# Optimization experiments

Hardware: AMD Instinct MI355X
Metric: run time of the kernel (lower is better)

The kernel has to match this reference:

```python
import jax, jax.numpy as jnp
import numpy as np

N = 100_000   # nodes
E = 3_200_000 # directed edges (avg degree 32)
D = 256       # feature dim (in_channels)
K = 2         # k of k-MIS


def _propagate_min(min_rank, row, col, n, k):
    # k iterations of scatter_min along edges (row -> col), keeping current value
    for _ in range(k):
        neigh = jax.ops.segment_min(min_rank[row], col, num_segments=n)
        min_rank = jnp.minimum(min_rank, neigh)
    return min_rank


def maximal_k_independent_set(row, col, rank, n, k):
    # Luby-style greedy k-MIS: repeatedly add nodes whose rank is minimal in their
    # k-hop in-neighbourhood, then mark (cover) the k-hop neighbourhood of the MIS.
    def dilate(mask):
        for _ in range(k):
            neigh = jax.ops.segment_max(mask[row].astype(jnp.int32), col, num_segments=n)
            mask = mask | (neigh > 0)
        return mask

    def cond(state):
        _, mask, _ = state
        return ~jnp.all(mask)

    def body(state):
        mis, mask, min_rank = state
        min_rank = _propagate_min(min_rank, row, col, n, k)
        mis = mis | (rank == min_rank)
        mask = dilate(mis)
        min_rank = jnp.where(mask, n, rank)  # covered nodes get rank 'infinity' (= n)
        return mis, mask, min_rank

    z = jnp.zeros((n,), dtype=bool)
    mis, _, _ = jax.lax.while_loop(cond, body, (z, z, rank))
    return mis


def cluster_k_mis(mis, row, col, rank, n, k):
    # min_rank = n everywhere except MIS nodes get their rank; propagate min k hops;
    # cluster id = index of the unique MIS rank each node ends up attached to.
    min_rank = jnp.where(mis, rank, n)
    min_rank = _propagate_min(min_rank, row, col, n, k)
    _, clusters = jnp.unique(min_rank, return_inverse=True)
    return clusters.reshape(-1).astype(jnp.int32)


def setup_inputs():
    key = jax.random.key(0)
    k1, k2, k3 = jax.random.split(key, 3)
    x = jax.random.normal(k1, (N, D), dtype=jnp.float32)
    edge_index = jax.random.randint(k2, (2, E), 0, N, dtype=jnp.int32)
    edge_attr = jax.random.normal(k3, (E,), dtype=jnp.float32)
    return {"x": x, "edge_index": edge_index, "edge_attr": edge_attr}


def reference(x, edge_index, edge_attr):
    n = x.shape[0]
    row, col = edge_index[0], edge_index[1]
    # scorer=None -> score = arange(n); greedy ordering of arange -> rank = arange(n)
    rank = jnp.arange(n, dtype=jnp.int32)

    mis = maximal_k_independent_set(row, col, rank, n, K)
    cluster = cluster_k_mis(mis, row, col, rank, n, K)
    c = int(mis.sum())  # number of clusters (MIS size)

    # --- pooled adjacency: coalesce duplicate (cluster[row], cluster[col]) with sum ---
    cl_np = np.asarray(cluster).astype(np.int64)
    r = cl_np[np.asarray(row)]
    cc = cl_np[np.asarray(col)]
    keys = r * np.int64(c) + cc
    uniq, inv = np.unique(keys, return_inverse=True)
    val = jax.ops.segment_sum(edge_attr, jnp.asarray(inv.astype(np.int32)),
                              num_segments=int(uniq.shape[0]))
    new_row = (uniq // c).astype(np.int32)
    new_col = (uniq % c).astype(np.int32)
    keep = np.nonzero(new_row != new_col)[0]  # remove_self_loops=True
    pooled_edge_index = jnp.stack([jnp.asarray(new_row[keep]), jnp.asarray(new_col[keep])])
    pooled_edge_attr = val[jnp.asarray(keep)]

    # --- pooled node features: reduce_x='sum' (adaptive=False, so no score scaling) ---
    x_pooled = jax.ops.segment_sum(x, cluster, num_segments=c)
    return x_pooled, pooled_edge_index, pooled_edge_attr
```

## Files before the change

kernel.cpp:

```cpp
#include <hip/hip_runtime.h>
#include <cmath>
#include <cstdint>

#define NT 256
#define EG0 1024
#define EG1 256
#define MAX_ROUND 16
#define KCOPY 4
#define SCAN_T 32
#define SCAN_IPB (NT*SCAN_T)
#define SENT 0x80000000u


__device__ __forceinline__ int getbit(const unsigned int* bm, int v){
  return (bm[v>>5]>>(v&31))&1u;
}
__device__ __forceinline__ void setbit(unsigned int* bm, int v){
  unsigned int m = 1u<<(v&31);
  if(!(bm[v>>5]&m)) atomicOr(&bm[v>>5], m);
}

__device__ __forceinline__ int block_append(int* cursor, bool pred, int* s_w){
  int wid  = threadIdx.x >> 6;
  int lane = threadIdx.x & 63;
  unsigned long long m = __ballot(pred);
  int cnt = __popcll(m);
  if(lane==0) s_w[wid]=cnt;
  __syncthreads();
  if(threadIdx.x==0){
    int t0=s_w[0], t1=s_w[1], t2=s_w[2], t3=s_w[3];
    int tot=t0+t1+t2+t3;
    int base = tot ? atomicAdd(cursor, tot) : 0;
    s_w[0]=base; s_w[1]=base+t0; s_w[2]=base+t0+t1; s_w[3]=base+t0+t1+t2;
  }
  __syncthreads();
  int pos = s_w[wid] + __popcll(m & ((1ull<<lane)-1ull));
  __syncthreads();
  return pos;
}


__global__ void k_init(int* a, int* b, int n){
  int v = blockIdx.x*NT + threadIdx.x;
  if(v<n){ a[v]=v; b[v]=v; }
}

__global__ void k_fill_dense(float* dcopies, const int* scal, long CMsq){
  long c = scal[0];
  long M = c*c; if(M>CMsq) M=CMsq;
  long stride = (long)gridDim.x*NT;
  for(long i = (long)blockIdx.x*NT + threadIdx.x; i<M; i+=stride){
    #pragma unroll
    for(int k=0;k<KCOPY;k++)
      ((unsigned int*)dcopies)[(long)k*CMsq + i] = SENT;
  }
}


__global__ void k_hop0(int* b, const int* __restrict__ row,
                       const int* __restrict__ col, int E){
  int stride = gridDim.x*NT;
  for(int e = blockIdx.x*NT + threadIdx.x; e<E; e+=stride){
    int s = row[e];
    if(s < b[col[e]]) atomicMin(&b[col[e]], s);
  }
}

__global__ void k_hop0f(int* a, const int* b, const int* __restrict__ row,
                        const int* __restrict__ col, int n, int E){
  int stride = gridDim.x*NT;
  int total = n + E;
  for(int i = blockIdx.x*NT + threadIdx.x; i<total; i+=stride){
    if(i<n){
      if(b[i] < a[i]) atomicMin(&a[i], b[i]);
    } else {
      int e = i-n;
      int s = b[row[e]];
      if(s < a[col[e]]) atomicMin(&a[col[e]], s);
    }
  }
}

__global__ void k_dil0(const int* a, int* d2, int* cover, const int* __restrict__ row,
                       const int* __restrict__ col, int E, int ep){
  int stride = gridDim.x*NT;
  for(int e = blockIdx.x*NT + threadIdx.x; e<E; e+=stride){
    int r = row[e];
    if(a[r]==r){
      int cc = col[e];
      d2[r]=ep;  cover[r]=1;
      d2[cc]=ep; cover[cc]=1;
    }
  }
}

__global__ void k_dil20(const int* a, const int* d2, int* cover, const int* __restrict__ row,
                        const int* __restrict__ col, int E, int ep){
  int stride = gridDim.x*NT;
  for(int e = blockIdx.x*NT + threadIdx.x; e<E; e+=stride){
    int r = row[e];
    if((d2[r]==ep || a[r]==r) && !cover[col[e]]) cover[col[e]]=1;
  }
}

__global__ void k_fincomp0(int* a, int* b, unsigned int* misb, int* cover, int n,
                           const int* __restrict__ row, const int* __restrict__ col, int E,
                           int2* Ld, int* lcnt1, int* U1, int* rcnt0){
  __shared__ int s_w[4];
  long nth = (long)gridDim.x*NT;
  for(long base = (long)blockIdx.x*NT; base < n; base += nth){
    int v = (int)base + threadIdx.x;
    bool unc = false;
    if(v<n){
      int nw = (a[v]==v);
      if(nw){ setbit(misb,v); if(!cover[v]) cover[v]=1; }
      int cov = cover[v] | nw;
      int val = cov ? n : v;
      a[v]=val; b[v]=val;
      unc = !cov;
    }
    int pos = block_append(rcnt0, unc, s_w);
    if(unc) U1[pos]=v;
  }
  for(long base = (long)blockIdx.x*NT; base < E; base += nth){
    int e = (int)base + threadIdx.x;
    bool keep=false; int2 ed;
    if(e<E){
      ed = make_int2(row[e], col[e]);
      keep = (!cover[ed.x]) || (!cover[ed.y]);
    }
    int pos = block_append(lcnt1, keep, s_w);
    if(keep) Ld[pos]=ed;
  }
}


__global__ void k_hop1(int* b, const int* a, const int2* L, const int* pE,
                       const int* gate){
  if(*gate==0) return;
  int E = *pE;
  int stride = gridDim.x*NT;
  for(int e = blockIdx.x*NT + threadIdx.x; e<E; e+=stride){
    int2 ed = L[e];
    int s = a[ed.x];
    if(s < b[ed.y]) atomicMin(&b[ed.y], s);
  }
}

__global__ void k_hop1f(int* a, const int* b, const int2* L, const int* pE,
                        const int* U, const int* pU, const int* gate){
  if(*gate==0) return;
  int E = *pE, un = *pU;
  int total = un + E;
  int stride = gridDim.x*NT;
  for(int i = blockIdx.x*NT + threadIdx.x; i<total; i+=stride){
    if(i<un){
      int u = U[i];
      if(b[u] < a[u]) atomicMin(&a[u], b[u]);
    } else {
      int2 ed = L[i-un];
      int s = b[ed.x];
      if(s < a[ed.y]) atomicMin(&a[ed.y], s);
    }
  }
}

__global__ void k_dil11(const int* a, int* d2, int* cover, unsigned int* misb,
                        const int2* L, const int* pE, const int* U, const int* pU,
                        const int* gate, int ep){
  if(*gate==0) return;
  int E = *pE, un = *pU;
  int total = un + E;
  int stride = gridDim.x*NT;
  for(int i = blockIdx.x*NT + threadIdx.x; i<total; i+=stride){
    if(i<un){
      int u = U[i];
      if(a[u]==u){ setbit(misb,u); cover[u]=1; d2[u]=ep; }
    } else {
      int2 ed = L[i-un];
      if(a[ed.x]==ed.x){ d2[ed.x]=ep; cover[ed.x]=1; d2[ed.y]=ep; cover[ed.y]=1; }
    }
  }
}

__global__ void k_dil21(const int* a, const int* d2, int* cover, const int2* L,
                        const int* pE, const int* gate, int ep){
  if(*gate==0) return;
  int E = *pE;
  int stride = gridDim.x*NT;
  for(int e = blockIdx.x*NT + threadIdx.x; e<E; e+=stride){
    int2 ed = L[e];
    if((d2[ed.x]==ep || a[ed.x]==ed.x) && !cover[ed.y]) cover[ed.y]=1;
  }
}

__global__ void k_fincomp1(int* a, int* b, const int* cover, int n,
                           const int2* Ls, const int* pE, int2* Ld, int* lcntD,
                           const int* Us, const int* pU, int* Ud, int* rcntD,
                           const int* gate){
  if(*gate==0) return;
  __shared__ int s_w[4];
  int E = *pE, un = *pU;
  long nth = (long)gridDim.x*NT;
  for(long base = (long)blockIdx.x*NT; base < un; base += nth){
    int i = (int)base + threadIdx.x;
    bool unc=false; int u=0;
    if(i<un){ u = Us[i]; unc = !cover[u]; }
    int pos = block_append(rcntD, unc, s_w);
    if(unc) Ud[pos]=u;
  }
  for(long base = (long)blockIdx.x*NT; base < E; base += nth){
    int e = (int)base + threadIdx.x;
    bool keep=false; int2 ed;
    if(e<E){
      ed = Ls[e];
      int vx = cover[ed.x] ? n : ed.x;  a[ed.x]=vx; b[ed.x]=vx;
      int vy = cover[ed.y] ? n : ed.y;  a[ed.y]=vy; b[ed.y]=vy;
      keep = (!cover[ed.x]) || (!cover[ed.y]);
    }
    int pos = block_append(lcntD, keep, s_w);
    if(keep) Ld[pos]=ed;
  }
}


__global__ void k_cluster_init(const unsigned int* misb, unsigned int* reach1b,
                               int* a, int* b, int n){
  int v = blockIdx.x*NT + threadIdx.x;
  if(v<n){
    int m = getbit(misb,v);
    int val = m ? v : n;
    a[v]=val; b[v]=val;
    if(m) setbit(reach1b,v);
  }
}

__global__ void k_chop1(int* b, const unsigned int* misb, unsigned int* reach1b,
                        const int* __restrict__ row, const int* __restrict__ col, int E){
  int stride = gridDim.x*NT;
  for(int e = blockIdx.x*NT + threadIdx.x; e<E; e+=stride){
    int r = row[e];
    if(getbit(misb,r)){
      int cc = col[e];
      if(r < b[cc]) atomicMin(&b[cc], r);
      setbit(reach1b, cc);
    }
  }
}

__global__ void k_chop2f(int* a, const int* b, const unsigned int* reach1b,
                         const int* __restrict__ row, const int* __restrict__ col,
                         int n, int E){
  int stride = gridDim.x*NT;
  int total = n + E;
  for(int i = blockIdx.x*NT + threadIdx.x; i<total; i+=stride){
    if(i<n){
      if(b[i] < a[i]) atomicMin(&a[i], b[i]);
    } else {
      int e = i-n;
      int r = row[e];
      if(getbit(reach1b,r)){
        int s = b[r];
        if(s < n && s < a[col[e]]) atomicMin(&a[col[e]], s);
      }
    }
  }
}

__global__ void k_mark(const int* mr, const unsigned int* misb, int* present, int* cmis, int n){
  int v = blockIdx.x*NT + threadIdx.x;
  int m = 0;
  if(v<n){
    int r = mr[v];
    if(r<n && !present[r]) present[r]=1;
    m = getbit(misb,v);
  }
  __shared__ int sh[NT];
  sh[threadIdx.x]=m; __syncthreads();
  for(int off=NT/2; off>0; off>>=1){
    if(threadIdx.x<off) sh[threadIdx.x]+=sh[threadIdx.x+off];
    __syncthreads();
  }
  if(threadIdx.x==0 && sh[0]) atomicAdd(cmis, sh[0]);
}


__global__ void k_scan1(const int* A, int M, int* bsum){
  int t = threadIdx.x;
  long base = (long)blockIdx.x*SCAN_IPB + (long)t*SCAN_T;
  int s = 0;
  #pragma unroll
  for(int j=0;j<SCAN_T;j++){ long i=base+j; if(i<M) s += A[i]; }
  __shared__ int sh[NT];
  sh[t]=s; __syncthreads();
  for(int off=NT/2; off>0; off>>=1){ if(t<off) sh[t]+=sh[t+off]; __syncthreads(); }
  if(t==0) bsum[blockIdx.x]=sh[0];
}

__global__ void k_scan2(const int* bsum, int* bscan, int B, int* totalOut){
  __shared__ int sh[NT];
  int t = threadIdx.x;
  int carry = 0;
  for(int base=0; base<B; base+=NT){
    int i = base+t;
    int v = (i<B) ? bsum[i] : 0;
    sh[t]=v; __syncthreads();
    for(int off=1; off<NT; off<<=1){
      int x=0; if(t>=off) x=sh[t-off];
      __syncthreads();
      sh[t]+=x; __syncthreads();
    }
    int incl = sh[t];
    if(i<B) bscan[i] = carry + incl - v;
    carry += sh[NT-1];
    __syncthreads();
  }
  if(t==0 && totalOut) *totalOut = carry;
}

__global__ void k_scan3(const int* A, int M, const int* bscan, int* pref){
  int t = threadIdx.x;
  long base = (long)blockIdx.x*SCAN_IPB + (long)t*SCAN_T;
  int s = 0;
  #pragma unroll
  for(int j=0;j<SCAN_T;j++){ long i=base+j; if(i<M) s += A[i]; }
  __shared__ int sh[NT];
  sh[t]=s; __syncthreads();
  for(int off=1; off<NT; off<<=1){
    int x=0; if(t>=off) x=sh[t-off];
    __syncthreads();
    sh[t]+=x; __syncthreads();
  }
  int run = bscan[blockIdx.x] + (sh[t]-s);
  for(int j=0;j<SCAN_T;j++){
    long i=base+j;
    if(i<M){ pref[i]=run; run += A[i]; }
  }
}


__global__ void k_assign(const int* mr, const int* pref, int* cl, int* ccount, int n){
  int v = blockIdx.x*NT + threadIdx.x;
  if(v<n){
    int r = mr[v];
    int cid = (r<n) ? pref[r] : 0;
    cl[v]=cid;
    atomicAdd(&ccount[cid],1);
  }
}

__global__ void k_scatter_nodes(const int* cl, const int* cstart, int* cursor, int* nodeList, int n){
  int v = blockIdx.x*NT + threadIdx.x;
  if(v<n){
    int cid = cl[v];
    int pos = cstart[cid] + atomicAdd(&cursor[cid],1);
    nodeList[pos]=v;
  }
}

__global__ void k_pool_x(const float* __restrict__ x, const int* nodeList, const int* cstart,
                         const int* ccount, const int* scal, float* out, long out_size){
  int c = scal[0], U = scal[1];
  int t = threadIdx.x;
  for(int cid=blockIdx.x; cid<c; cid+=gridDim.x){
    float s0=0.f, s1=0.f, s2=0.f, s3=0.f;
    if(cid<U){
      int st = cstart[cid], cn = ccount[cid];
      int i=0;
      for(; i+3<cn; i+=4){
        int n0=nodeList[st+i], n1=nodeList[st+i+1], n2=nodeList[st+i+2], n3=nodeList[st+i+3];
        s0 += x[(size_t)n0*256 + t];
        s1 += x[(size_t)n1*256 + t];
        s2 += x[(size_t)n2*256 + t];
        s3 += x[(size_t)n3*256 + t];
      }
      for(; i<cn; i++) s0 += x[(size_t)nodeList[st+i]*256 + t];
      s0 += s1+s2+s3;
    }
    long idx = (long)cid*256 + t;
    if(idx < out_size) out[idx]=s0;
  }
}

__global__ void k_edge_pool(const int* __restrict__ row, const int* __restrict__ col,
                            const float* __restrict__ attr, const int* cl,
                            const int* scal, float* dcopies, int E, long CMsq){
  int c = scal[0];
  float* dc = dcopies + (long)(blockIdx.x & (KCOPY-1))*CMsq;
  int stride = gridDim.x*NT;
  for(int e = blockIdx.x*NT + threadIdx.x; e<E; e+=stride){
    long key = (long)cl[row[e]]*c + cl[col[e]];
    if(key < CMsq){
      unsafeAtomicAdd(&dc[key], attr[e]);
    }
  }
}

__global__ void k_reduce_dense(const float* __restrict__ dcopies, float* dense,
                               const int* scal, long CMsq){
  long c = scal[0];
  long M = c*c; if(M>CMsq) M=CMsq;
  long stride = (long)gridDim.x*NT;
  for(long i = (long)blockIdx.x*NT + threadIdx.x; i<M; i+=stride){
    float s = dcopies[i];
    #pragma unroll
    for(int k=1;k<KCOPY;k++) s += dcopies[(long)k*CMsq + i];
    dense[i]=s;
  }
}

__device__ __forceinline__ int cellp(const float* dense, long i){
  return __float_as_uint(dense[i]) != SENT;
}

__global__ void k_cscan1(const float* dense, const int* scal, int* bsum, long CMsq){
  int c = scal[0];
  long M = (long)c*c; if(M>CMsq) M=CMsq;
  int t = threadIdx.x;
  long base = (long)blockIdx.x*SCAN_IPB + (long)t*SCAN_T;
  int s = 0;
  if(base < M && c > 0){
    int r = (int)(base / c);
    int q = (int)(base - (long)r*c);
    for(int j=0;j<SCAN_T;j++){
      long i=base+j;
      if(i<M){
        if(cellp(dense,i) && r!=q) s++;
      }
      if(++q==c){ q=0; r++; }
    }
  }
  __shared__ int sh[NT];
  sh[t]=s; __syncthreads();
  for(int off=NT/2; off>0; off>>=1){ if(t<off) sh[t]+=sh[t+off]; __syncthreads(); }
  if(t==0) bsum[blockIdx.x]=sh[0];
}

__global__ void k_cemit(const float* dense, const int* scal,
                        const int* bscan, float* out, long out_size, long CMsq){
  int c = scal[0]; int P = scal[2];
  long M = (long)c*c; if(M>CMsq) M=CMsq;
  long xoff = (long)c*256;
  int t = threadIdx.x;
  long base = (long)blockIdx.x*SCAN_IPB + (long)t*SCAN_T;
  int s = 0;
  int r0=0,q0=0;
  if(base < M && c > 0){
    r0 = (int)(base / c);
    q0 = (int)(base - (long)r0*c);
    int r=r0, q=q0;
    for(int j=0;j<SCAN_T;j++){
      long i=base+j;
      if(i<M){
        if(cellp(dense,i) && r!=q) s++;
      }
      if(++q==c){ q=0; r++; }
    }
  }
  __shared__ int sh[NT];
  sh[t]=s; __syncthreads();
  for(int off=1; off<NT; off<<=1){
    int x=0; if(t>=off) x=sh[t-off];
    __syncthreads();
    sh[t]+=x; __syncthreads();
  }
  int run = bscan[blockIdx.x] + (sh[t]-s);
  if(base < M && c > 0){
    int r=r0, q=q0;
    for(int j=0;j<SCAN_T;j++){
      long i=base+j;
      if(i<M && cellp(dense,i) && r!=q){
        long o0 = xoff + run;
        long o1 = xoff + (long)P + run;
        long o2 = xoff + 2L*(long)P + run;
        if(o0<out_size) out[o0]=(float)r;
        if(o1<out_size) out[o1]=(float)q;
        if(o2<out_size) out[o2]=dense[i];
        run++;
      }
      if(++q==c){ q=0; r++; }
    }
  }
}


extern "C" void kernel_launch(void* const* d_in, const int* in_sizes, int n_in,
                              void* d_out, int out_size, void* d_ws, size_t ws_size,
                              hipStream_t stream){
  (void)n_in;
  const float* x     = (const float*)d_in[0];
  const int*   eidx  = (const int*)d_in[1];
  const float* eattr = (const float*)d_in[2];
  const int D = 256;
  int n = in_sizes[0]/D;
  int E = in_sizes[1]/2;
  const int* row = eidx;
  const int* col = eidx + E;
  int nwords = (n+31)>>5;
  int CU_B = out_size/256 + 1; if(CU_B > n) CU_B = n;

  char* p = (char*)d_ws;
  auto alloc = [&](size_t bytes)->char*{ char* r=p; p += (bytes+255)&~(size_t)255; return r; };
  int2* LA   = (int2*)alloc((size_t)E*8);
  int2* LB   = (int2*)alloc((size_t)E*8);
  int* a     = (int*)alloc((size_t)n*4);
  int* b     = (int*)alloc((size_t)n*4);
  int* cl    = (int*)alloc((size_t)n*4);
  int* nodeList = (int*)alloc((size_t)n*4);
  int* pref  = (int*)alloc((size_t)n*4);
  int* U1    = (int*)alloc((size_t)n*4);
  int* U2    = (int*)alloc((size_t)n*4);
  int* bsum  = (int*)alloc(4096*4);
  int* bscan = (int*)alloc(4096*4);
  char* zstart = p;
  int* cover   = (int*)alloc((size_t)n*4);
  int* d2      = (int*)alloc((size_t)n*4);
  unsigned int* misb    = (unsigned int*)alloc((size_t)nwords*4);
  unsigned int* reach1b = (unsigned int*)alloc((size_t)nwords*4);
  int* present = (int*)alloc((size_t)n*4);
  int* ccount  = (int*)alloc((size_t)n*4);
  int* cursor  = (int*)alloc((size_t)n*4);
  int* rcnt    = (int*)alloc((MAX_ROUND+2)*4);
  int* lcnt    = (int*)alloc((MAX_ROUND+2)*4);
  int* scal    = (int*)alloc(64);
  size_t zbytes = (size_t)(p - zstart);

  size_t used   = (size_t)(p-(char*)d_ws);
  size_t remain = (ws_size > used+4096) ? ws_size-used-4096 : 0;
  size_t maxcells = remain/(4*(KCOPY+1));
  long CM = CU_B;
  while(CM>1 && (size_t)CM*CM > maxcells) CM--;
  long CMsq = CM*CM;
  float* dcopies = (float*)alloc((size_t)KCOPY*CMsq*4);
  float* dense   = (float*)alloc((size_t)CMsq*4);

  hipMemsetAsync(zstart, 0, zbytes, stream);

  int NB  = (n+NT-1)/NT;
  int NBs = (n+SCAN_IPB-1)/SCAN_IPB;
  int NBc = (CU_B+SCAN_IPB-1)/SCAN_IPB;
  int CB  = (int)((CMsq+SCAN_IPB-1)/SCAN_IPB);
  if(CB>4096) CB=4096;

  k_init    <<<NB,NT,0,stream>>>(a,b,n);
  k_hop0    <<<EG0,NT,0,stream>>>(b,row,col,E);
  k_hop0f   <<<EG0,NT,0,stream>>>(a,b,row,col,n,E);
  k_dil0    <<<EG0,NT,0,stream>>>(a,d2,cover,row,col,E,1);
  k_dil20   <<<EG0,NT,0,stream>>>(a,d2,cover,row,col,E,1);
  k_fincomp0<<<EG0,NT,0,stream>>>(a,b,misb,cover,n,row,col,E,LB,&lcnt[1],U1,&rcnt[0]);

  for(int r=1; r<MAX_ROUND; ++r){
    int2* Ls = (r&1) ? LB : LA;
    int2* Ld = (r&1) ? LA : LB;
    int*  Us = (r&1) ? U1 : U2;
    int*  Ud = (r&1) ? U2 : U1;
    int ep = r+1;
    k_hop1    <<<EG1,NT,0,stream>>>(b,a,Ls,&lcnt[r],&rcnt[r-1]);
    k_hop1f   <<<EG1,NT,0,stream>>>(a,b,Ls,&lcnt[r],Us,&rcnt[r-1],&rcnt[r-1]);
    k_dil11   <<<EG1,NT,0,stream>>>(a,d2,cover,misb,Ls,&lcnt[r],Us,&rcnt[r-1],&rcnt[r-1],ep);
    k_dil21   <<<EG1,NT,0,stream>>>(a,d2,cover,Ls,&lcnt[r],&rcnt[r-1],ep);
    k_fincomp1<<<EG1,NT,0,stream>>>(a,b,cover,n,Ls,&lcnt[r],Ld,&lcnt[r+1],
                                    Us,&rcnt[r-1],Ud,&rcnt[r],&rcnt[r-1]);
  }

  k_cluster_init<<<NB,NT,0,stream>>>(misb,reach1b,a,b,n);
  k_chop1 <<<EG0,NT,0,stream>>>(b,misb,reach1b,row,col,E);
  k_chop2f<<<EG0,NT,0,stream>>>(a,b,reach1b,row,col,n,E);

  k_mark <<<NB,NT,0,stream>>>(a,misb,present,scal,n);
  k_scan1<<<NBs,NT,0,stream>>>(present,n,bsum);
  k_scan2<<<1,NT,0,stream>>>(bsum,bscan,NBs,scal+1);
  k_scan3<<<NBs,NT,0,stream>>>(present,n,bscan,pref);
  k_assign<<<NB,NT,0,stream>>>(a,pref,cl,ccount,n);

  k_fill_dense<<<2048,NT,0,stream>>>(dcopies,scal,CMsq);

  k_scan1<<<NBc,NT,0,stream>>>(ccount,CU_B,bsum);
  k_scan2<<<1,NT,0,stream>>>(bsum,bscan,NBc,nullptr);
  k_scan3<<<NBc,NT,0,stream>>>(ccount,CU_B,bscan,pref);
  k_scatter_nodes<<<NB,NT,0,stream>>>(cl,pref,cursor,nodeList,n);

  k_pool_x<<<1024,NT,0,stream>>>(x,nodeList,pref,ccount,scal,(float*)d_out,(long)out_size);

  k_edge_pool<<<EG0,NT,0,stream>>>(row,col,eattr,cl,scal,dcopies,E,CMsq);
  k_reduce_dense<<<1024,NT,0,stream>>>(dcopies,dense,scal,CMsq);
  k_cscan1<<<CB,NT,0,stream>>>(dense,scal,bsum,CMsq);
  k_scan2 <<<1,NT,0,stream>>>(bsum,bscan,CB,scal+2);
  k_cemit <<<CB,NT,0,stream>>>(dense,scal,bscan,(float*)d_out,(long)out_size,CMsq);
}
```

Before: 1.823 ms.

## Split pooled-x sum into four segments per cluster and size dense-copy count dynamically

The node-feature pooling now gives each cluster four blocks, each summing a quarter of the cluster's nodes with eight independent accumulators. The partial sums go to a scratch buffer and a second kernel adds them into the output. This exposes more parallelism for large clusters. The number of privatized dense edge-accumulator copies is now derived from the remaining workspace (capped at eight) rather than fixed at four, which spreads the float atomics over more copies but raises the fill and reduce traffic.

After: 1.730 ms. 1.05x faster.

```diff
diff --git a/kernel.cpp b/kernel.cpp
--- a/kernel.cpp
+++ b/kernel.cpp
@@ -6,7 +6,6 @@
 #define EG0 1024
 #define EG1 256
 #define MAX_ROUND 16
-#define KCOPY 4
 #define SCAN_T 32
 #define SCAN_IPB (NT*SCAN_T)
 #define SENT 0x80000000u
@@ -45,13 +44,12 @@
   if(v<n){ a[v]=v; b[v]=v; }
 }
 
-__global__ void k_fill_dense(float* dcopies, const int* scal, long CMsq){
+__global__ void k_fill_dense(float* dcopies, const int* scal, long CMsq, int KC){
   long c = scal[0];
   long M = c*c; if(M>CMsq) M=CMsq;
   long stride = (long)gridDim.x*NT;
   for(long i = (long)blockIdx.x*NT + threadIdx.x; i<M; i+=stride){
-    #pragma unroll
-    for(int k=0;k<KCOPY;k++)
+    for(int k=0;k<KC;k++)
       ((unsigned int*)dcopies)[(long)k*CMsq + i] = SENT;
   }
 }
@@ -358,35 +356,50 @@
   }
 }
 
-__global__ void k_pool_x(const float* __restrict__ x, const int* nodeList, const int* cstart,
-                         const int* ccount, const int* scal, float* out, long out_size){
+__global__ void k_pool_seg(const float* __restrict__ x, const int* nodeList, const int* cstart,
+                           const int* ccount, const int* scal, float* part, long partStride){
   int c = scal[0], U = scal[1];
   int t = threadIdx.x;
-  for(int cid=blockIdx.x; cid<c; cid+=gridDim.x){
-    float s0=0.f, s1=0.f, s2=0.f, s3=0.f;
+  int total = c*4;
+  for(int idx = blockIdx.x; idx < total; idx += gridDim.x){
+    int cid = idx>>2, seg = idx&3;
+    float s0=0.f,s1=0.f,s2=0.f,s3=0.f,s4=0.f,s5=0.f,s6=0.f,s7=0.f;
     if(cid<U){
       int st = cstart[cid], cn = ccount[cid];
-      int i=0;
-      for(; i+3<cn; i+=4){
-        int n0=nodeList[st+i], n1=nodeList[st+i+1], n2=nodeList[st+i+2], n3=nodeList[st+i+3];
-        s0 += x[(size_t)n0*256 + t];
-        s1 += x[(size_t)n1*256 + t];
-        s2 += x[(size_t)n2*256 + t];
-        s3 += x[(size_t)n3*256 + t];
+      int q  = (cn+3)>>2;
+      int lo = seg*q, hi = lo+q; if(hi>cn) hi=cn;
+      int i=lo;
+      for(; i+7<hi; i+=8){
+        int n0=nodeList[st+i],   n1=nodeList[st+i+1], n2=nodeList[st+i+2], n3=nodeList[st+i+3];
+        int n4=nodeList[st+i+4], n5=nodeList[st+i+5], n6=nodeList[st+i+6], n7=nodeList[st+i+7];
+        s0 += x[(size_t)n0*256 + t]; s1 += x[(size_t)n1*256 + t];
+        s2 += x[(size_t)n2*256 + t]; s3 += x[(size_t)n3*256 + t];
+        s4 += x[(size_t)n4*256 + t]; s5 += x[(size_t)n5*256 + t];
+        s6 += x[(size_t)n6*256 + t]; s7 += x[(size_t)n7*256 + t];
       }
-      for(; i<cn; i++) s0 += x[(size_t)nodeList[st+i]*256 + t];
-      s0 += s1+s2+s3;
-    }
-    long idx = (long)cid*256 + t;
-    if(idx < out_size) out[idx]=s0;
+      for(; i<hi; i++) s0 += x[(size_t)nodeList[st+i]*256 + t];
+      s0 += s1+s2+s3+s4+s5+s6+s7;
+    }
+    part[(long)seg*partStride + (long)cid*256 + t] = s0;
+  }
+}
+
+__global__ void k_pool_add(const float* __restrict__ part, long partStride,
+                           const int* scal, float* out, long out_size){
+  int c = scal[0];
+  long M = (long)c*256;
+  long stride = (long)gridDim.x*NT;
+  for(long i = (long)blockIdx.x*NT + threadIdx.x; i<M; i+=stride){
+    float s = part[i] + part[partStride+i] + part[2L*partStride+i] + part[3L*partStride+i];
+    if(i < out_size) out[i]=s;
   }
 }
 
 __global__ void k_edge_pool(const int* __restrict__ row, const int* __restrict__ col,
                             const float* __restrict__ attr, const int* cl,
-                            const int* scal, float* dcopies, int E, long CMsq){
+                            const int* scal, float* dcopies, int E, long CMsq, int KC){
   int c = scal[0];
-  float* dc = dcopies + (long)(blockIdx.x & (KCOPY-1))*CMsq;
+  float* dc = dcopies + (long)(blockIdx.x % KC)*CMsq;
   int stride = gridDim.x*NT;
   for(int e = blockIdx.x*NT + threadIdx.x; e<E; e+=stride){
     long key = (long)cl[row[e]]*c + cl[col[e]];
@@ -397,14 +410,13 @@
 }
 
 __global__ void k_reduce_dense(const float* __restrict__ dcopies, float* dense,
-                               const int* scal, long CMsq){
+                               const int* scal, long CMsq, int KC){
   long c = scal[0];
   long M = c*c; if(M>CMsq) M=CMsq;
   long stride = (long)gridDim.x*NT;
   for(long i = (long)blockIdx.x*NT + threadIdx.x; i<M; i+=stride){
     float s = dcopies[i];
-    #pragma unroll
-    for(int k=1;k<KCOPY;k++) s += dcopies[(long)k*CMsq + i];
+    for(int k=1;k<KC;k++) s += dcopies[(long)k*CMsq + i];
     dense[i]=s;
   }
 }
@@ -525,13 +537,21 @@
   int* scal    = (int*)alloc(64);
   size_t zbytes = (size_t)(p - zstart);
 
+  long partStride = (long)CU_B*256;
+  float* part = (float*)alloc((size_t)4*partStride*4);
+
   size_t used   = (size_t)(p-(char*)d_ws);
   size_t remain = (ws_size > used+4096) ? ws_size-used-4096 : 0;
-  size_t maxcells = remain/(4*(KCOPY+1));
   long CM = CU_B;
-  while(CM>1 && (size_t)CM*CM > maxcells) CM--;
   long CMsq = CM*CM;
-  float* dcopies = (float*)alloc((size_t)KCOPY*CMsq*4);
+  int KC = (int)(remain/(4*(size_t)CMsq)) - 1;
+  if(KC > 8) KC = 8;
+  if(KC < 1){
+    KC = 1;
+    while(CM>1 && (size_t)(KC+1)*CM*CM*4 > remain) CM--;
+    CMsq = CM*CM;
+  }
+  float* dcopies = (float*)alloc((size_t)KC*CMsq*4);
   float* dense   = (float*)alloc((size_t)CMsq*4);
 
   hipMemsetAsync(zstart, 0, zbytes, stream);
@@ -573,17 +593,18 @@
   k_scan3<<<NBs,NT,0,stream>>>(present,n,bscan,pref);
   k_assign<<<NB,NT,0,stream>>>(a,pref,cl,ccount,n);
 
-  k_fill_dense<<<2048,NT,0,stream>>>(dcopies,scal,CMsq);
+  k_fill_dense<<<2048,NT,0,stream>>>(dcopies,scal,CMsq,KC);
 
   k_scan1<<<NBc,NT,0,stream>>>(ccount,CU_B,bsum);
   k_scan2<<<1,NT,0,stream>>>(bsum,bscan,NBc,nullptr);
   k_scan3<<<NBc,NT,0,stream>>>(ccount,CU_B,bscan,pref);
   k_scatter_nodes<<<NB,NT,0,stream>>>(cl,pref,cursor,nodeList,n);
 
-  k_pool_x<<<1024,NT,0,stream>>>(x,nodeList,pref,ccount,scal,(float*)d_out,(long)out_size);
-
-  k_edge_pool<<<EG0,NT,0,stream>>>(row,col,eattr,cl,scal,dcopies,E,CMsq);
-  k_reduce_dense<<<1024,NT,0,stream>>>(dcopies,dense,scal,CMsq);
+  k_pool_seg<<<2048,NT,0,stream>>>(x,nodeList,pref,ccount,scal,part,partStride);
+  k_pool_add<<<256,NT,0,stream>>>(part,partStride,scal,(float*)d_out,(long)out_size);
+
+  k_edge_pool<<<EG0,NT,0,stream>>>(row,col,eattr,cl,scal,dcopies,E,CMsq,KC);
+  k_reduce_dense<<<1024,NT,0,stream>>>(dcopies,dense,scal,CMsq,KC);
   k_cscan1<<<CB,NT,0,stream>>>(dense,scal,bsum,CMsq);
   k_scan2 <<<1,NT,0,stream>>>(bsum,bscan,CB,scal+2);
   k_cemit <<<CB,NT,0,stream>>>(dense,scal,bscan,(float*)d_out,(long)out_size,CMsq);
```
